# Kernel optimization log

Measured on AMD Instinct MI355X. Metric: run time of the kernel, lower is better.

The kernel has to match this reference:

```python
import jax, jax.numpy as jnp
import numpy as np

B, N, D = 8, 4096, 3


def setup_inputs() -> dict:
    key = jax.random.key(0)
    k1, k2 = jax.random.split(key)
    array1 = jax.random.normal(k1, (B, N, D), dtype=jnp.float32)
    array2 = jax.random.normal(k2, (B, N, D), dtype=jnp.float32)
    return {"array1": array1, "array2": array2}


def reference(array1, array2):
    # Pairwise squared distances: sq[b, i, j] = ||array1[b,i] - array2[b,j]||^2
    diff = array1[:, :, None, :] - array2[:, None, :, :]   # [B, N1, N2, D]
    sq = jnp.sum(diff * diff, axis=-1)                     # [B, N1, N2]
    # array2samples_distance(a1, a2): for each point of a2, min dist to a1, then mean
    av_dist1 = jnp.mean(jnp.min(sq, axis=1), axis=-1)      # [B] (min over array1 points)
    # array2samples_distance(a2, a1): for each point of a1, min dist to a2, then mean
    av_dist2 = jnp.mean(jnp.min(sq, axis=2), axis=-1)      # [B] (min over array2 points)
    dist1 = jnp.mean(av_dist1)
    dist2 = jnp.mean(av_dist2)
    dist_all = dist1 + dist2
    return (dist_all, dist1, dist2)
```

## Files before the change

kernel.cpp:

```cpp
#include <hip/hip_runtime.h>

#define BB 8
#define NN 4096
#define THREADS 256
#define NSPLIT 16
#define CHUNK (NN / NSPLIT)
#define NPAIR (CHUNK / 2)
#define QPT 8
#define QPB (THREADS * QPT)
#define NQ (BB * NN)
#define NQ_TOTAL (2 * NQ)

typedef float v2f __attribute__((ext_vector_type(2)));

template <int SEL>
__device__ __forceinline__ v2f pk3(v2f X2, v2f Y2, v2f Z2, v2f W2,
                                   v2f qx, v2f qy, v2f qz) {
    v2f t;
    if constexpr (SEL == 0) {
        asm("v_pk_fma_f32 %0, %1, %2, %3 op_sel:[0,0,0] op_sel_hi:[1,0,1]"
            : "=v"(t) : "v"(Z2), "v"(qz), "v"(W2));
        asm("v_pk_fma_f32 %0, %1, %2, %0 op_sel:[0,0,0] op_sel_hi:[1,0,1]"
            : "+v"(t) : "v"(Y2), "v"(qy));
        asm("v_pk_fma_f32 %0, %1, %2, %0 op_sel:[0,0,0] op_sel_hi:[1,0,1]"
            : "+v"(t) : "v"(X2), "v"(qx));
    } else {
        asm("v_pk_fma_f32 %0, %1, %2, %3 op_sel:[0,1,0] op_sel_hi:[1,1,1]"
            : "=v"(t) : "v"(Z2), "v"(qz), "v"(W2));
        asm("v_pk_fma_f32 %0, %1, %2, %0 op_sel:[0,1,0] op_sel_hi:[1,1,1]"
            : "+v"(t) : "v"(Y2), "v"(qy));
        asm("v_pk_fma_f32 %0, %1, %2, %0 op_sel:[0,1,0] op_sel_hi:[1,1,1]"
            : "+v"(t) : "v"(X2), "v"(qx));
    }
    return t;
}

__global__ __launch_bounds__(THREADS) void chamfer_min_kernel(
    const float* __restrict__ a1, const float* __restrict__ a2,
    float* __restrict__ minpart)
{
    __shared__ float4 sdb4[2 * NPAIR];

    const int tid = threadIdx.x;
    const int bid = blockIdx.x;
    const int c   = bid & (NSPLIT - 1);
    const int qb  = (bid >> 4) & 1;
    const int b   = (bid >> 5) & 7;
    const int dir = bid >> 8;

    const float* dbg = (dir == 0 ? a1 : a2) + (size_t)b * NN * 3;
    const float* qg  = (dir == 0 ? a2 : a1) + (size_t)b * NN * 3;

    if (tid < NPAIR) {
        const float2* s2 = reinterpret_cast<const float2*>(dbg + (size_t)c * CHUNK * 3);
        const float2 u = s2[3 * tid + 0];
        const float2 v = s2[3 * tid + 1];
        const float2 w = s2[3 * tid + 2];
        const float w0 = 0.5f * fmaf(u.x, u.x, fmaf(u.y, u.y, v.x * v.x));
        const float w1 = 0.5f * fmaf(v.y, v.y, fmaf(w.x, w.x, w.y * w.y));
        sdb4[2 * tid]     = make_float4(u.x, v.y, u.y, w.x);
        sdb4[2 * tid + 1] = make_float4(v.x, w.y, w0, w1);
    }

    v2f qc0[QPT / 2], qc1[QPT / 2], qc2[QPT / 2];
    {
        const float4* q4 = reinterpret_cast<const float4*>(
            qg + (size_t)(qb * QPB + tid * QPT) * 3);
        const float4 v0 = q4[0], v1 = q4[1], v2 = q4[2];
        const float4 v3 = q4[3], v4 = q4[4], v5 = q4[5];
        qc0[0] = (v2f){-v0.x, -v0.w};  qc1[0] = (v2f){-v0.y, -v1.x};  qc2[0] = (v2f){-v0.z, -v1.y};
        qc0[1] = (v2f){-v1.z, -v2.y};  qc1[1] = (v2f){-v1.w, -v2.z};  qc2[1] = (v2f){-v2.x, -v2.w};
        qc0[2] = (v2f){-v3.x, -v3.w};  qc1[2] = (v2f){-v3.y, -v4.x};  qc2[2] = (v2f){-v3.z, -v4.y};
        qc0[3] = (v2f){-v4.z, -v5.y};  qc1[3] = (v2f){-v4.w, -v5.z};  qc2[3] = (v2f){-v5.x, -v5.w};
    }

    __syncthreads();

    float m[QPT];
    #pragma unroll
    for (int k = 0; k < QPT; ++k) m[k] = 3.4e38f;

    float4 A0 = sdb4[0], B0 = sdb4[1];
    float4 A1 = sdb4[2], B1 = sdb4[3];
    for (int ip = 0; ip < NPAIR - 2; ip += 2) {
        const float4 nA0 = sdb4[2 * ip + 4];
        const float4 nB0 = sdb4[2 * ip + 5];
        const float4 nA1 = sdb4[2 * ip + 6];
        const float4 nB1 = sdb4[2 * ip + 7];
        {
            const v2f X2 = (v2f){A0.x, A0.y}, Y2 = (v2f){A0.z, A0.w};
            const v2f Z2 = (v2f){B0.x, B0.y}, W2 = (v2f){B0.z, B0.w};
            #pragma unroll
            for (int k2 = 0; k2 < QPT / 2; ++k2) {
                const v2f t0 = pk3<0>(X2, Y2, Z2, W2, qc0[k2], qc1[k2], qc2[k2]);
                m[2 * k2]     = fminf(fminf(t0[0], t0[1]), m[2 * k2]);
                const v2f t1 = pk3<1>(X2, Y2, Z2, W2, qc0[k2], qc1[k2], qc2[k2]);
                m[2 * k2 + 1] = fminf(fminf(t1[0], t1[1]), m[2 * k2 + 1]);
            }
        }
        {
            const v2f X2 = (v2f){A1.x, A1.y}, Y2 = (v2f){A1.z, A1.w};
            const v2f Z2 = (v2f){B1.x, B1.y}, W2 = (v2f){B1.z, B1.w};
            #pragma unroll
            for (int k2 = 0; k2 < QPT / 2; ++k2) {
                const v2f t0 = pk3<0>(X2, Y2, Z2, W2, qc0[k2], qc1[k2], qc2[k2]);
                m[2 * k2]     = fminf(fminf(t0[0], t0[1]), m[2 * k2]);
                const v2f t1 = pk3<1>(X2, Y2, Z2, W2, qc0[k2], qc1[k2], qc2[k2]);
                m[2 * k2 + 1] = fminf(fminf(t1[0], t1[1]), m[2 * k2 + 1]);
            }
        }
        A0 = nA0; B0 = nB0; A1 = nA1; B1 = nB1;
    }
    #pragma unroll
    for (int rep = 0; rep < 2; ++rep) {
        const float4 A = rep ? A1 : A0;
        const float4 Bv = rep ? B1 : B0;
        const v2f X2 = (v2f){A.x, A.y}, Y2 = (v2f){A.z, A.w};
        const v2f Z2 = (v2f){Bv.x, Bv.y}, W2 = (v2f){Bv.z, Bv.w};
        #pragma unroll
        for (int k2 = 0; k2 < QPT / 2; ++k2) {
            const v2f t0 = pk3<0>(X2, Y2, Z2, W2, qc0[k2], qc1[k2], qc2[k2]);
            m[2 * k2]     = fminf(fminf(t0[0], t0[1]), m[2 * k2]);
            const v2f t1 = pk3<1>(X2, Y2, Z2, W2, qc0[k2], qc1[k2], qc2[k2]);
            m[2 * k2 + 1] = fminf(fminf(t1[0], t1[1]), m[2 * k2 + 1]);
        }
    }

    float4 o0, o1;
    o0.x = m[0]; o0.y = m[1]; o0.z = m[2]; o0.w = m[3];
    o1.x = m[4]; o1.y = m[5]; o1.z = m[6]; o1.w = m[7];

    const size_t qglob = (size_t)dir * NQ + (size_t)b * NN + (size_t)(qb * QPB + tid * QPT);
    float4* dst = reinterpret_cast<float4*>(minpart + (size_t)c * NQ_TOTAL + qglob);
    dst[0] = o0;
    dst[1] = o1;
}

__global__ __launch_bounds__(THREADS) void decode_sum_kernel(
    const float* __restrict__ a1, const float* __restrict__ a2,
    const float* __restrict__ minpart, float* __restrict__ partials)
{
    __shared__ float red[THREADS];
    const int tid = threadIdx.x;
    const int bid = blockIdx.x;
    const int gq  = bid * THREADS + tid;
    const int dir = gq >> 15;
    const int b   = (gq >> 12) & 7;
    const int q   = gq & (NN - 1);

    float mn = 3.4e38f;
    #pragma unroll
    for (int cc = 0; cc < NSPLIT; ++cc)
        mn = fminf(mn, minpart[(size_t)cc * NQ_TOTAL + gq]);

    const float* qp = (dir == 0 ? a2 : a1) + ((size_t)b * NN + q) * 3;
    const float qx = qp[0], qy = qp[1], qz = qp[2];
    const float qn = fmaf(qx, qx, fmaf(qy, qy, qz * qz));
    const float d  = fmaf(2.0f, mn, qn);

    red[tid] = d;
    __syncthreads();
    #pragma unroll
    for (int s = THREADS / 2; s > 0; s >>= 1) {
        if (tid < s) red[tid] += red[tid + s];
        __syncthreads();
    }
    if (tid == 0) partials[bid] = red[0];
}

__global__ __launch_bounds__(256) void finalize_kernel(
    const float* __restrict__ partials, float* __restrict__ out)
{
    __shared__ float red[256];
    const int t = threadIdx.x;
    red[t] = partials[t];
    __syncthreads();
    #pragma unroll
    for (int s = 64; s > 0; s >>= 1) {
        if ((t & 127) < s) red[t] += red[t + s];
        __syncthreads();
    }
    if (t == 0) {
        const float inv = 1.0f / (float)(BB * NN);
        const float d1 = red[0]   * inv;
        const float d2 = red[128] * inv;
        out[0] = d1 + d2;
        out[1] = d1;
        out[2] = d2;
    }
}

extern "C" void kernel_launch(void* const* d_in, const int* in_sizes, int n_in,
                              void* d_out, int out_size, void* d_ws, size_t ws_size,
                              hipStream_t stream)
{
    const float* a1 = (const float*)d_in[0];
    const float* a2 = (const float*)d_in[1];
    float* out = (float*)d_out;

    float* minpart  = (float*)d_ws;
    float* partials = (float*)((char*)d_ws + (size_t)NSPLIT * NQ_TOTAL * sizeof(float));

    hipLaunchKernelGGL(chamfer_min_kernel, dim3(2 * BB * 2 * NSPLIT), dim3(THREADS), 0, stream,
                       a1, a2, minpart);
    hipLaunchKernelGGL(decode_sum_kernel, dim3(NQ_TOTAL / THREADS), dim3(THREADS), 0, stream,
                       a1, a2, minpart, partials);
    hipLaunchKernelGGL(finalize_kernel, dim3(1), dim3(256), 0, stream,
                       partials, out);
}
```

Measured before the change: 33.19 us.

## Precompute packed database in a prep kernel and read it directly from global memory

Adds a separate prep kernel that packs each database chunk into float4 pairs with half-norms once, and removes the per-block LDS staging and __syncthreads from the main distance kernel. The main loop now reads the packed data straight from global memory through uniform addresses that hit the scalar or vector caches. This removes the redundant per-block packing (each chunk was packed twice) and the barrier, at the cost of an extra kernel launch, a global write and read of the packed buffer, and possibly higher load latency in the inner loop than LDS.

```diff
diff --git a/kernel.cpp b/kernel.cpp
--- a/kernel.cpp
+++ b/kernel.cpp
@@ -10,6 +10,8 @@
 #define QPB (THREADS * QPT)
 #define NQ (BB * NN)
 #define NQ_TOTAL (2 * NQ)
+#define PAIRS_PER_DB (NN / 2)
+#define PAIRS_TOTAL (2 * BB * PAIRS_PER_DB)
 
 typedef float v2f __attribute__((ext_vector_type(2)));
 
@@ -35,12 +37,31 @@
     return t;
 }
 
+__global__ __launch_bounds__(THREADS) void prep_kernel(
+    const float* __restrict__ a1, const float* __restrict__ a2,
+    float4* __restrict__ pkdb)
+{
+    const int gid  = blockIdx.x * THREADS + threadIdx.x;
+    const int dir  = gid >> 14;
+    const int b    = (gid >> 11) & 7;
+    const int pair = gid & (PAIRS_PER_DB - 1);
+
+    const float* src = (dir == 0 ? a1 : a2) + (size_t)b * NN * 3;
+    const float2* s2 = reinterpret_cast<const float2*>(src);
+    const float2 u = s2[3 * pair + 0];
+    const float2 v = s2[3 * pair + 1];
+    const float2 w = s2[3 * pair + 2];
+    const float w0 = 0.5f * fmaf(u.x, u.x, fmaf(u.y, u.y, v.x * v.x));
+    const float w1 = 0.5f * fmaf(v.y, v.y, fmaf(w.x, w.x, w.y * w.y));
+    float4* dst = pkdb + (size_t)2 * gid;
+    dst[0] = make_float4(u.x, v.y, u.y, w.x);
+    dst[1] = make_float4(v.x, w.y, w0, w1);
+}
+
 __global__ __launch_bounds__(THREADS) void chamfer_min_kernel(
     const float* __restrict__ a1, const float* __restrict__ a2,
-    float* __restrict__ minpart)
-{
-    __shared__ float4 sdb4[2 * NPAIR];
-
+    const float4* __restrict__ pkdb, float* __restrict__ minpart)
+{
     const int tid = threadIdx.x;
     const int bid = blockIdx.x;
     const int c   = bid & (NSPLIT - 1);
@@ -48,19 +69,9 @@
     const int b   = (bid >> 5) & 7;
     const int dir = bid >> 8;
 
-    const float* dbg = (dir == 0 ? a1 : a2) + (size_t)b * NN * 3;
-    const float* qg  = (dir == 0 ? a2 : a1) + (size_t)b * NN * 3;
-
-    if (tid < NPAIR) {
-        const float2* s2 = reinterpret_cast<const float2*>(dbg + (size_t)c * CHUNK * 3);
-        const float2 u = s2[3 * tid + 0];
-        const float2 v = s2[3 * tid + 1];
-        const float2 w = s2[3 * tid + 2];
-        const float w0 = 0.5f * fmaf(u.x, u.x, fmaf(u.y, u.y, v.x * v.x));
-        const float w1 = 0.5f * fmaf(v.y, v.y, fmaf(w.x, w.x, w.y * w.y));
-        sdb4[2 * tid]     = make_float4(u.x, v.y, u.y, w.x);
-        sdb4[2 * tid + 1] = make_float4(v.x, w.y, w0, w1);
-    }
+    const float* qg = (dir == 0 ? a2 : a1) + (size_t)b * NN * 3;
+    const float4* gdb = pkdb +
+        ((size_t)(dir * BB + b) * PAIRS_PER_DB + (size_t)c * NPAIR) * 2;
 
     v2f qc0[QPT / 2], qc1[QPT / 2], qc2[QPT / 2];
     {
@@ -74,19 +85,17 @@
         qc0[3] = (v2f){-v4.z, -v5.y};  qc1[3] = (v2f){-v4.w, -v5.z};  qc2[3] = (v2f){-v5.x, -v5.w};
     }
 
-    __syncthreads();
-
     float m[QPT];
     #pragma unroll
     for (int k = 0; k < QPT; ++k) m[k] = 3.4e38f;
 
-    float4 A0 = sdb4[0], B0 = sdb4[1];
-    float4 A1 = sdb4[2], B1 = sdb4[3];
+    float4 A0 = gdb[0], B0 = gdb[1];
+    float4 A1 = gdb[2], B1 = gdb[3];
     for (int ip = 0; ip < NPAIR - 2; ip += 2) {
-        const float4 nA0 = sdb4[2 * ip + 4];
-        const float4 nB0 = sdb4[2 * ip + 5];
-        const float4 nA1 = sdb4[2 * ip + 6];
-        const float4 nB1 = sdb4[2 * ip + 7];
+        const float4 nA0 = gdb[2 * ip + 4];
+        const float4 nB0 = gdb[2 * ip + 5];
+        const float4 nA1 = gdb[2 * ip + 6];
+        const float4 nB1 = gdb[2 * ip + 7];
         {
             const v2f X2 = (v2f){A0.x, A0.y}, Y2 = (v2f){A0.z, A0.w};
             const v2f Z2 = (v2f){B0.x, B0.y}, W2 = (v2f){B0.z, B0.w};
@@ -113,7 +122,7 @@
     }
     #pragma unroll
     for (int rep = 0; rep < 2; ++rep) {
-        const float4 A = rep ? A1 : A0;
+        const float4 A  = rep ? A1 : A0;
         const float4 Bv = rep ? B1 : B0;
         const v2f X2 = (v2f){A.x, A.y}, Y2 = (v2f){A.z, A.w};
         const v2f Z2 = (v2f){Bv.x, Bv.y}, W2 = (v2f){Bv.z, Bv.w};
@@ -198,11 +207,14 @@
     const float* a2 = (const float*)d_in[1];
     float* out = (float*)d_out;
 
-    float* minpart  = (float*)d_ws;
-    float* partials = (float*)((char*)d_ws + (size_t)NSPLIT * NQ_TOTAL * sizeof(float));
-
+    float4* pkdb    = (float4*)d_ws;
+    float*  minpart = (float*)((char*)d_ws + (size_t)PAIRS_TOTAL * 2 * sizeof(float4));
+    float*  partials = minpart + (size_t)NSPLIT * NQ_TOTAL;
+
+    hipLaunchKernelGGL(prep_kernel, dim3(PAIRS_TOTAL / THREADS), dim3(THREADS), 0, stream,
+                       a1, a2, pkdb);
     hipLaunchKernelGGL(chamfer_min_kernel, dim3(2 * BB * 2 * NSPLIT), dim3(THREADS), 0, stream,
-                       a1, a2, minpart);
+                       a1, a2, pkdb, minpart);
     hipLaunchKernelGGL(decode_sum_kernel, dim3(NQ_TOTAL / THREADS), dim3(THREADS), 0, stream,
                        a1, a2, minpart, partials);
     hipLaunchKernelGGL(finalize_kernel, dim3(1), dim3(256), 0, stream,
```

Measured after the change: 46.07 us. 38.8% more time.
